# Performance work log

Measured on AMD Instinct MI355X. Metric: run time of the kernel, lower is better.

Reference implementation:

```python
import jax, jax.numpy as jnp
import numpy as np

B, D, NR, H = 8, 64, 6, 3        # batch, input_dim, num_relation, num_hop
R2 = 2 * NR                      # relations incl. inverses
NUM_RULE = R2 ** H               # 1728 combinatorial rules
EPS = 1e-6
TAU = 1.0


def _rule_indices():
    # torch.meshgrid (indexing='ij') over num_hop copies of arange(2*NR), stacked on last dim
    a = np.arange(R2)
    grids = np.meshgrid(*([a] * H), indexing="ij")
    return jnp.asarray(np.stack(grids, -1).reshape(-1, H))  # [NUM_RULE, H] int


def setup_inputs() -> dict:
    key = jax.random.key(0)
    ks = jax.random.split(key, 11)
    s = 0.1
    return {
        "query": jax.random.normal(ks[0], (B, D), jnp.float32),
        "relation_emb": jax.random.normal(ks[1], (R2, D), jnp.float32) * s,      # nn.Embedding(2*NR, D)
        "indicator": jax.random.normal(ks[2], (D,), jnp.float32) * s,            # nn.Embedding(1, D)
        "rel_W": jax.random.normal(ks[3], (H, D, R2 * D), jnp.float32) * s,      # per-layer relation_linear
        "rel_b": jax.random.normal(ks[4], (H, R2 * D), jnp.float32) * s,
        "lin_W": jax.random.normal(ks[5], (H, 13 * D, D), jnp.float32) * s,      # per-layer combine Linear(13D->D)
        "lin_b": jax.random.normal(ks[6], (H, D), jnp.float32) * s,
        "mlp_W1": jax.random.normal(ks[7], (2 * D, D), jnp.float32) * s,
        "mlp_b1": jax.random.normal(ks[8], (D,), jnp.float32) * s,
        "mlp_W2": jax.random.normal(ks[9], (D, 1), jnp.float32) * s,
        "mlp_b2": jax.random.normal(ks[10], (1,), jnp.float32) * s,
    }


def reference(query, relation_emb, indicator, rel_W, rel_b, lin_W, lin_b,
              mlp_W1, mlp_b1, mlp_W2, mlp_b2):
    rel_idx = _rule_indices()                       # [R, H]
    Rn = rel_idx.shape[0]

    # PNA degree scales: each graph is a chain; degree_out+1 (boundary self-message)
    # node 0 -> 1 message (boundary only), nodes 1..H -> 2 messages (edge + boundary)
    log_deg_head = jnp.log(jnp.float32(1.0))
    log_deg_tail = jnp.log(jnp.float32(2.0))
    mean_scale = (log_deg_head + H * log_deg_tail) / (H + 1)
    s_head = log_deg_head / mean_scale
    s_tail = log_deg_tail / mean_scale
    scales_head = jnp.stack([jnp.float32(1.0), s_head, 1.0 / jnp.maximum(s_head, 1e-2)])
    scales_tail = jnp.stack([jnp.float32(1.0), s_tail, 1.0 / jnp.maximum(s_tail, 1e-2)])

    # node-0 PNA update: single message == boundary == indicator (constant across graphs)
    # stats layout per feature dim: (mean, max, min, std)
    f0 = jnp.stack([indicator, indicator, indicator,
                    jnp.full((D,), float(np.sqrt(EPS)), indicator.dtype)], -1).reshape(4 * D)
    upd0 = (f0[:, None] * scales_head).reshape(12 * D)

    # boundary / initial hidden: indicator at node 0 of every graph
    hidden = jnp.zeros((B, Rn, H + 1, D), query.dtype)
    hidden = hidden.at[:, :, 0, :].set(indicator)

    for l in range(H):
        # dependent relation table from the query (relation_linear)
        rel_table = (query @ rel_W[l] + rel_b[l]).reshape(B, R2, D)
        rel = rel_table[:, rel_idx]                 # [B, R, H, D] gather per edge
        msg = hidden[:, :, :-1, :] * rel            # distmult message on edges h -> h+1
        # tail-node PNA stats over message set {msg, boundary=0}
        mean = msg * 0.5
        mx = jnp.maximum(msg, 0.0)
        mn = jnp.minimum(msg, 0.0)
        std = jnp.sqrt(jnp.maximum(msg * msg * 0.25, EPS))   # sq_mean - mean^2 = msg^2/4
        feats = jnp.stack([mean, mx, mn, std], -1).reshape(B, Rn, H, 4 * D)
        upd_tail = (feats[..., None] * scales_tail).reshape(B, Rn, H, 12 * D)
        upd = jnp.concatenate(
            [jnp.broadcast_to(upd0, (B, Rn, 1, 12 * D)), upd_tail], axis=2)
        # combine: relu(Linear(cat([input, update])))
        hidden = jax.nn.relu(
            jnp.concatenate([hidden, upd], -1) @ lin_W[l] + lin_b[l])

    # readout at tail node H, concat per-node query
    feat = jnp.concatenate(
        [hidden[:, :, H, :], jnp.broadcast_to(query[:, None, :], (B, Rn, D))], -1)
    score = (jax.nn.relu(feat @ mlp_W1 + mlp_b1) @ mlp_W2 + mlp_b2)[..., 0]   # [B, R]
    attention = jax.nn.softmax(score / TAU, axis=-1)
    r_emb = relation_emb[rel_idx]                   # [R, H, D]
    subgoals = jnp.einsum("br,rhd->bhd", attention, r_emb)
    masks = jnp.ones((B, H), bool)
    return subgoals, masks
```

## Files before the change

### kernel.cpp

```cpp
#include <hip/hip_runtime.h>
#include <hip/hip_bf16.h>


typedef const float* fp;

#define WS_WT     0
#define WS_RELT   49152
#define WS_QW1    67584
#define WS_Q2     68096
#define WS_QW3    141824
#define WS_SCORES 142592

__device__ __forceinline__ void accq(float4 mv, float4 tv,
                                     float4 wa, float4 wb, float4 wc, float4 wd,
                                     float& acc){
  acc += mv.x*wa.x; acc += fabsf(mv.x)*wa.y; acc += tv.x*wa.z;
  acc += mv.y*wb.x; acc += fabsf(mv.y)*wb.y; acc += tv.y*wb.z;
  acc += mv.z*wc.x; acc += fabsf(mv.z)*wc.y; acc += tv.z*wc.z;
  acc += mv.w*wd.x; acc += fabsf(mv.w)*wd.y; acc += tv.w*wd.z;
}

__global__ void k_pre1(fp lin_W, fp query, fp rel_W, fp rel_b, fp mlp_W1,
                       fp mlp_b1, float* ws){
  int t = blockIdx.x*256 + threadIdx.x;
  if (t < 49152){
    int c = t & 3; int j = (t>>2)&63; int d = (t>>8)&63; int l = t>>14;
    fp W = lin_W + (size_t)l*832*64 + (64 + 12*d)*64 + j;
    float v = 0.f;
    if (c == 0){
      float w0 = W[0]   + (4.f/3.f)*W[64]  + 0.75f*W[128];
      float w1 = W[192] + (4.f/3.f)*W[256] + 0.75f*W[320];
      float w2 = W[384] + (4.f/3.f)*W[448] + 0.75f*W[512];
      v = 0.5f*w0 + 0.5f*(w1 + w2);
    } else if (c == 1){
      float w1 = W[192] + (4.f/3.f)*W[256] + 0.75f*W[320];
      float w2 = W[384] + (4.f/3.f)*W[448] + 0.75f*W[512];
      v = 0.5f*(w1 - w2);
    } else if (c == 2){
      v = 0.5f*(W[576] + (4.f/3.f)*W[640] + 0.75f*W[704]);
    }
    ws[WS_WT + t] = v;
  } else if (t < 67584){
    int e = t - 49152;
    int d = e & 63; int j = (e>>6)%12; int b = (e/768)&7; int l = e/6144;
    float acc = rel_b[l*768 + j*64 + d];
    fp W = rel_W + (size_t)l*64*768 + j*64 + d;
    fp q = query + b*64;
    #pragma unroll 32
    for (int k=0;k<64;k++) acc += q[k] * W[k*768];
    ws[WS_RELT + e] = acc;
  } else if (t < 68096){
    int e = t - 67584; int b = e>>6; int j = e&63;
    float acc = mlp_b1[j];
    fp q = query + b*64;
    #pragma unroll 32
    for (int i=0;i<64;i++) acc += q[i] * mlp_W1[(64+i)*64 + j];
    ws[WS_QW1 + e] = acc;
  }
}

__global__ void k_mid(fp indicator, fp lin_W, fp lin_b, float* ws){
  __shared__ float sC2[64], sC2W[64], sP1[64], sQ3[12][64];
  __shared__ __align__(16) float mP[64], tP[64];
  __shared__ __align__(16) float mL[12][64], tL[12][64];
  int tid = threadIdx.x;
  int w = tid>>6, j = tid&63;
  bool isQ2 = blockIdx.x < 96;
  int b  = isQ2 ? blockIdx.x/12 : blockIdx.x-96;
  int i0 = isQ2 ? blockIdx.x%12 : 0;
  if (w == 0){
    float acc = lin_b[j];
    #pragma unroll 8
    for (int d=0; d<64; d++) acc += 2e-3f * ws[WS_WT + ((d<<6)+j)*4 + 2];
    sC2[j] = fmaxf(acc, 0.f);
  } else if (w == 1 && isQ2){
    const float* rel = ws + WS_RELT + (b*12+i0)*64;
    float m = indicator[j] * rel[j];
    mP[j] = m; tP[j] = fmaxf(fabsf(m), 2e-3f);
  }
  __syncthreads();
  if (w == 0){
    float a2 = lin_b[64+j];
    fp W1 = lin_W + 832*64;
    #pragma unroll 16
    for (int k=0;k<64;k++) a2 += sC2[k] * W1[k*64+j];
    sC2W[j] = a2;
  } else if (w == 1 && isQ2){
    const float4* W4 = (const float4*)(ws + WS_WT);
    float acc = lin_b[j];
    #pragma unroll
    for (int dq=0; dq<16; dq++){
      float4 mv = ((const float4*)mP)[dq], tv = ((const float4*)tP)[dq];
      float4 wa = W4[(dq*4+0)*64+j], wb = W4[(dq*4+1)*64+j],
             wc = W4[(dq*4+2)*64+j], wd = W4[(dq*4+3)*64+j];
      accq(mv,tv,wa,wb,wc,wd,acc);
    }
    sP1[j] = fmaxf(acc, 0.f);
  }
  __syncthreads();
  {
    const float* rel = ws + WS_RELT + 6144 + (b*12+w)*64;
    float s = isQ2 ? sP1[j] : sC2[j];
    float m = s * rel[j];
    mL[w][j] = m; tL[w][j] = fmaxf(fabsf(m), 2e-3f);
  }
  __syncthreads();
  const float4* W4 = (const float4*)(ws + WS_WT + 16384);
  float acc = sC2W[j];
  #pragma unroll
  for (int dq=0; dq<16; dq++){
    float4 mv = ((const float4*)mL[w])[dq], tv = ((const float4*)tL[w])[dq];
    float4 wa = W4[(dq*4+0)*64+j], wb = W4[(dq*4+1)*64+j],
           wc = W4[(dq*4+2)*64+j], wd = W4[(dq*4+3)*64+j];
    accq(mv,tv,wa,wb,wc,wd,acc);
  }
  if (isQ2){
    ws[WS_Q2 + ((b*12+i0)*12+w)*64 + j] = fmaxf(acc, 0.f);
  } else {
    sQ3[w][j] = fmaxf(acc, 0.f);
    __syncthreads();
    fp W2 = lin_W + 2*832*64;
    float a = lin_b[128+j];
    #pragma unroll 16
    for (int k=0;k<64;k++) a += sQ3[w][k]*W2[k*64+j];
    ws[WS_QW3 + (b*12+w)*64 + j] = a;
  }
}

__global__ __launch_bounds__(256) void k_score(fp mlp_W1, fp mlp_W2, float* ws){
  __shared__ float wt_s[4096];
  __shared__ float fin[4][4][64];
  __shared__ __align__(16) float m_s[4][4][64];
  __shared__ __align__(16) float t_s[4][4][64];
  int tid = threadIdx.x, w = tid>>6, j = tid&63;
  int wave = blockIdx.x*4 + w;
  int b = blockIdx.x/108;
  int rem = wave%432;
  int i0 = rem/36; int t36 = rem%36;
  int i2 = t36/3;  int i1b = (t36%3)*4;
  {
    float rl = ws[WS_RELT + 12288 + (b*12+i2)*64 + j];
    #pragma unroll
    for (int r=0;r<4;r++){
      float qv = ws[WS_Q2 + ((b*12+i0)*12 + i1b + r)*64 + j];
      float m = qv*rl;
      m_s[w][r][j] = m;
      t_s[w][r][j] = fmaxf(fabsf(m), 2e-3f);
    }
  }
  float a0 = ws[WS_QW3 + (b*12+i2)*64 + j];
  float acc[4] = {a0, a0, a0, a0};
  const float4* Wt2 = (const float4*)(ws + WS_WT + 32768);
  for (int ch=0; ch<4; ch++){
    __syncthreads();
    {
      const float4* src = Wt2 + ch*1024;
      float4* dst = (float4*)wt_s;
      #pragma unroll
      for (int k=0; k<4; k++) dst[tid + k*256] = src[tid + k*256];
    }
    __syncthreads();
    #pragma unroll
    for (int dq=0; dq<4; dq++){
      int dc = ch*4 + dq;
      const float4* wl = (const float4*)wt_s + dq*256 + j;
      float4 wa = wl[0], wb = wl[64], wc = wl[128], wd = wl[192];
      #pragma unroll
      for (int r=0;r<4;r++){
        float4 mv = ((const float4*)m_s[w][r])[dc];
        float4 tv = ((const float4*)t_s[w][r])[dc];
        accq(mv,tv,wa,wb,wc,wd,acc[r]);
      }
    }
  }
  __syncthreads();
  fin[w][0][j]=fmaxf(acc[0],0.f); fin[w][1][j]=fmaxf(acc[1],0.f);
  fin[w][2][j]=fmaxf(acc[2],0.f); fin[w][3][j]=fmaxf(acc[3],0.f);
  __syncthreads();
  float qw = ws[WS_QW1 + b*64 + j];
  float w2v = mlp_W2[j];
  float h0=qw, h1=qw, h2=qw, h3=qw;
  #pragma unroll 8
  for (int i=0;i<64;i++){
    float wv = mlp_W1[i*64+j];
    h0 += fin[w][0][i]*wv; h1 += fin[w][1][i]*wv;
    h2 += fin[w][2][i]*wv; h3 += fin[w][3][i]*wv;
  }
  float s0=fmaxf(h0,0.f)*w2v, s1=fmaxf(h1,0.f)*w2v;
  float s2=fmaxf(h2,0.f)*w2v, s3=fmaxf(h3,0.f)*w2v;
  #pragma unroll
  for (int off=32; off>0; off>>=1){
    s0 += __shfl_down(s0, off, 64); s1 += __shfl_down(s1, off, 64);
    s2 += __shfl_down(s2, off, 64); s3 += __shfl_down(s3, off, 64);
  }
  if (j == 0){
    int rbase = i0*144 + i1b*12 + i2;
    float* S = ws + WS_SCORES + b*1728 + rbase;
    S[0] = s0; S[12] = s1; S[24] = s2; S[36] = s3;
  }
}

__global__ void k_final(fp relation_emb, float* ws, float* out){
  int b = blockIdx.x, tid = threadIdx.x;
  int w = tid>>6, lane = tid&63;
  __shared__ float se[1728];
  __shared__ float wred[4];
  __shared__ float pb[36][4];
  __shared__ float bins[36];
  const float* sc = ws + WS_SCORES + b*1728;
  float mx = -1e30f;
  for (int r=tid; r<1728; r+=256){ float v = sc[r]; se[r] = v; mx = fmaxf(mx, v); }
  #pragma unroll
  for (int off=32; off>0; off>>=1) mx = fmaxf(mx, __shfl_xor(mx, off, 64));
  if (lane == 0) wred[w] = mx;
  __syncthreads();
  mx = fmaxf(fmaxf(wred[0],wred[1]), fmaxf(wred[2],wred[3]));
  __syncthreads();
  float ts = 0.f;
  for (int r=tid; r<1728; r+=256){ float e = __expf(se[r]-mx); se[r] = e; ts += e; }
  #pragma unroll
  for (int off=32; off>0; off>>=1) ts += __shfl_xor(ts, off, 64);
  if (lane == 0) wred[w] = ts;
  __syncthreads();
  float tot = (wred[0]+wred[1]) + (wred[2]+wred[3]);
  if (tid < 144){
    int bin = tid>>2, q = tid&3;
    int h = bin/12, jj = bin%12;
    float a = 0.f;
    if (h == 0){
      const float* p = se + jj*144 + q*36;
      #pragma unroll 4
      for (int k=0;k<36;k++) a += p[k];
    } else if (h == 1){
      for (int t=q*36; t<q*36+36; t++) a += se[(t/12)*144 + jj*12 + (t%12)];
    } else {
      for (int t=q*36; t<q*36+36; t++) a += se[(t/12)*144 + (t%12)*12 + jj];
    }
    pb[bin][q] = a;
  }
  __syncthreads();
  if (tid < 36) bins[tid] = (pb[tid][0]+pb[tid][1]) + (pb[tid][2]+pb[tid][3]);
  __syncthreads();
  if (tid < 192){
    int h = tid>>6, d = tid&63;
    float acc = 0.f;
    #pragma unroll
    for (int jj=0; jj<12; jj++) acc += bins[h*12+jj] * relation_emb[jj*64+d];
    out[b*192 + tid] = acc/tot;
  }
  if (tid >= 192 && tid < 195){
    out[1536 + b*3 + (tid-192)] = 1.0f;
  }
}

extern "C" void kernel_launch(void* const* d_in, const int* in_sizes, int n_in,
                              void* d_out, int out_size, void* d_ws, size_t ws_size,
                              hipStream_t stream){
  fp query        = (fp)d_in[0];
  fp relation_emb = (fp)d_in[1];
  fp indicator    = (fp)d_in[2];
  fp rel_W        = (fp)d_in[3];
  fp rel_b        = (fp)d_in[4];
  fp lin_W        = (fp)d_in[5];
  fp lin_b        = (fp)d_in[6];
  fp mlp_W1       = (fp)d_in[7];
  fp mlp_b1       = (fp)d_in[8];
  fp mlp_W2       = (fp)d_in[9];
  float* ws = (float*)d_ws;
  float* out = (float*)d_out;

  k_pre1 <<<266, 256, 0, stream>>>(lin_W, query, rel_W, rel_b, mlp_W1, mlp_b1, ws);
  k_mid  <<<104, 768, 0, stream>>>(indicator, lin_W, lin_b, ws);
  k_score<<<864, 256, 0, stream>>>(mlp_W1, mlp_W2, ws);
  k_final<<<8,   256, 0, stream>>>(relation_emb, ws, out);
}
```

Before: 115.5 us.

## Fuse preprocessing and mid kernels, recomputing folded weights per block in LDS

Merges the weight-folding and relation-projection pre-kernel into the mid kernel. Each of the 104 mid blocks now recomputes the folded layer-0/1 weights (32K floats) and its own relation projections into shared memory, while 30 extra blocks produce the layer-2 data that later kernels still read from the workspace. This removes one launch and the global round trip between the two kernels. In exchange it adds redundant global reads and folding work in every block and uses 128KB of LDS per block, which limits occupancy.

After: 145.2 us. 1.26x slower.

```diff
diff --git a/kernel.cpp b/kernel.cpp
--- a/kernel.cpp
+++ b/kernel.cpp
@@ -20,62 +20,96 @@
   acc += mv.w*wd.x; acc += fabsf(mv.w)*wd.y; acc += tv.w*wd.z;
 }
 
-__global__ void k_pre1(fp lin_W, fp query, fp rel_W, fp rel_b, fp mlp_W1,
-                       fp mlp_b1, float* ws){
-  int t = blockIdx.x*256 + threadIdx.x;
-  if (t < 49152){
-    int c = t & 3; int j = (t>>2)&63; int d = (t>>8)&63; int l = t>>14;
-    fp W = lin_W + (size_t)l*832*64 + (64 + 12*d)*64 + j;
-    float v = 0.f;
-    if (c == 0){
-      float w0 = W[0]   + (4.f/3.f)*W[64]  + 0.75f*W[128];
-      float w1 = W[192] + (4.f/3.f)*W[256] + 0.75f*W[320];
-      float w2 = W[384] + (4.f/3.f)*W[448] + 0.75f*W[512];
-      v = 0.5f*w0 + 0.5f*(w1 + w2);
-    } else if (c == 1){
-      float w1 = W[192] + (4.f/3.f)*W[256] + 0.75f*W[320];
-      float w2 = W[384] + (4.f/3.f)*W[448] + 0.75f*W[512];
-      v = 0.5f*(w1 - w2);
-    } else if (c == 2){
-      v = 0.5f*(W[576] + (4.f/3.f)*W[640] + 0.75f*W[704]);
-    }
-    ws[WS_WT + t] = v;
-  } else if (t < 67584){
-    int e = t - 49152;
-    int d = e & 63; int j = (e>>6)%12; int b = (e/768)&7; int l = e/6144;
-    float acc = rel_b[l*768 + j*64 + d];
-    fp W = rel_W + (size_t)l*64*768 + j*64 + d;
+__device__ __forceinline__ float foldWt(fp lin_W, int l, int d, int j, int c){
+  fp W = lin_W + (size_t)l*832*64 + (64 + 12*d)*64 + j;
+  float v = 0.f;
+  if (c == 0){
+    float w0 = W[0]   + (4.f/3.f)*W[64]  + 0.75f*W[128];
+    float w1 = W[192] + (4.f/3.f)*W[256] + 0.75f*W[320];
+    float w2 = W[384] + (4.f/3.f)*W[448] + 0.75f*W[512];
+    v = 0.5f*w0 + 0.5f*(w1 + w2);
+  } else if (c == 1){
+    float w1 = W[192] + (4.f/3.f)*W[256] + 0.75f*W[320];
+    float w2 = W[384] + (4.f/3.f)*W[448] + 0.75f*W[512];
+    v = 0.5f*(w1 - w2);
+  } else if (c == 2){
+    v = 0.5f*(W[576] + (4.f/3.f)*W[640] + 0.75f*W[704]);
+  }
+  return v;
+}
+
+__global__ __launch_bounds__(768) void k_pre(fp indicator, fp query, fp lin_W,
+                       fp lin_b, fp rel_W, fp rel_b, fp mlp_W1, fp mlp_b1,
+                       float* ws){
+  __shared__ float sWt[32768];
+  __shared__ float sC2[64], sC2W[64], sP1[64], sQ3[12][64];
+  __shared__ __align__(16) float mP[64], tP[64];
+  __shared__ __align__(16) float mL[12][64], tL[12][64];
+  __shared__ __align__(16) float sRel0[64];
+  __shared__ __align__(16) float sRel1[12][64];
+  int tid = threadIdx.x;
+
+  if (blockIdx.x < 30){
+    int t = blockIdx.x*768 + tid;
+    if (t < 16384){
+      int g = 32768 + t;
+      int c = g & 3; int j = (g>>2)&63; int d = (g>>8)&63;
+      ws[WS_WT + g] = foldWt(lin_W, 2, d, j, c);
+    } else if (t < 22528){
+      int e = 12288 + (t - 16384);
+      int d = e & 63; int j = (e>>6)%12; int b = (e/768)&7;
+      float acc = rel_b[2*768 + j*64 + d];
+      fp W = rel_W + (size_t)2*64*768 + j*64 + d;
+      fp q = query + b*64;
+      #pragma unroll 32
+      for (int k=0;k<64;k++) acc += q[k] * W[k*768];
+      ws[WS_RELT + e] = acc;
+    } else if (t < 23040){
+      int e = t - 22528; int b = e>>6; int j = e&63;
+      float acc = mlp_b1[j];
+      fp q = query + b*64;
+      #pragma unroll 32
+      for (int i=0;i<64;i++) acc += q[i] * mlp_W1[(64+i)*64 + j];
+      ws[WS_QW1 + e] = acc;
+    }
+    return;
+  }
+
+  int mb = blockIdx.x - 30;
+  int w = tid>>6, j = tid&63;
+  bool isQ2 = mb < 96;
+  int b  = isQ2 ? mb/12 : mb-96;
+  int i0 = isQ2 ? mb%12 : 0;
+
+  for (int f = tid; f < 32768; f += 768){
+    int c = f & 3; int jj = (f>>2)&63; int d = (f>>8)&63; int l = f>>14;
+    sWt[f] = foldWt(lin_W, l, d, jj, c);
+  }
+  {
+    int idx = tid>>6, d = tid&63;
+    float acc = rel_b[768 + idx*64 + d];
+    fp W = rel_W + (size_t)64*768 + idx*64 + d;
     fp q = query + b*64;
     #pragma unroll 32
     for (int k=0;k<64;k++) acc += q[k] * W[k*768];
-    ws[WS_RELT + e] = acc;
-  } else if (t < 68096){
-    int e = t - 67584; int b = e>>6; int j = e&63;
-    float acc = mlp_b1[j];
+    sRel1[idx][d] = acc;
+  }
+  if (isQ2 && tid < 64){
+    float acc = rel_b[i0*64 + tid];
+    fp W = rel_W + i0*64 + tid;
     fp q = query + b*64;
     #pragma unroll 32
-    for (int i=0;i<64;i++) acc += q[i] * mlp_W1[(64+i)*64 + j];
-    ws[WS_QW1 + e] = acc;
-  }
-}
-
-__global__ void k_mid(fp indicator, fp lin_W, fp lin_b, float* ws){
-  __shared__ float sC2[64], sC2W[64], sP1[64], sQ3[12][64];
-  __shared__ __align__(16) float mP[64], tP[64];
-  __shared__ __align__(16) float mL[12][64], tL[12][64];
-  int tid = threadIdx.x;
-  int w = tid>>6, j = tid&63;
-  bool isQ2 = blockIdx.x < 96;
-  int b  = isQ2 ? blockIdx.x/12 : blockIdx.x-96;
-  int i0 = isQ2 ? blockIdx.x%12 : 0;
+    for (int k=0;k<64;k++) acc += q[k] * W[k*768];
+    sRel0[tid] = acc;
+  }
+  __syncthreads();
   if (w == 0){
     float acc = lin_b[j];
     #pragma unroll 8
-    for (int d=0; d<64; d++) acc += 2e-3f * ws[WS_WT + ((d<<6)+j)*4 + 2];
+    for (int d=0; d<64; d++) acc += 2e-3f * sWt[((d<<6)+j)*4 + 2];
     sC2[j] = fmaxf(acc, 0.f);
   } else if (w == 1 && isQ2){
-    const float* rel = ws + WS_RELT + (b*12+i0)*64;
-    float m = indicator[j] * rel[j];
+    float m = indicator[j] * sRel0[j];
     mP[j] = m; tP[j] = fmaxf(fabsf(m), 2e-3f);
   }
   __syncthreads();
@@ -86,7 +120,7 @@
     for (int k=0;k<64;k++) a2 += sC2[k] * W1[k*64+j];
     sC2W[j] = a2;
   } else if (w == 1 && isQ2){
-    const float4* W4 = (const float4*)(ws + WS_WT);
+    const float4* W4 = (const float4*)sWt;
     float acc = lin_b[j];
     #pragma unroll
     for (int dq=0; dq<16; dq++){
@@ -99,13 +133,12 @@
   }
   __syncthreads();
   {
-    const float* rel = ws + WS_RELT + 6144 + (b*12+w)*64;
     float s = isQ2 ? sP1[j] : sC2[j];
-    float m = s * rel[j];
+    float m = s * sRel1[w][j];
     mL[w][j] = m; tL[w][j] = fmaxf(fabsf(m), 2e-3f);
   }
   __syncthreads();
-  const float4* W4 = (const float4*)(ws + WS_WT + 16384);
+  const float4* W4 = (const float4*)(sWt + 16384);
   float acc = sC2W[j];
   #pragma unroll
   for (int dq=0; dq<16; dq++){
@@ -269,8 +302,8 @@
   float* ws = (float*)d_ws;
   float* out = (float*)d_out;
 
-  k_pre1 <<<266, 256, 0, stream>>>(lin_W, query, rel_W, rel_b, mlp_W1, mlp_b1, ws);
-  k_mid  <<<104, 768, 0, stream>>>(indicator, lin_W, lin_b, ws);
+  k_pre  <<<134, 768, 0, stream>>>(indicator, query, lin_W, lin_b, rel_W, rel_b,
+                                   mlp_W1, mlp_b1, ws);
   k_score<<<864, 256, 0, stream>>>(mlp_W1, mlp_W2, ws);
   k_final<<<8,   256, 0, stream>>>(relation_emb, ws, out);
 }
```

## Restructure k_pre1: stage lin_W in shared memory and split-K dot products

Applied to the files above, without the earlier changes.

The weight-folding part of k_pre1 now loads a contiguous lin_W slab into shared memory with float4 loads and computes the folded weights from LDS, instead of doing strided global reads per thread. The rel_W and mlp_W1 query projections are split over four K-chunks per block with a shared-memory reduction, shortening each thread's serial 64-long dot product and raising the block count. This preprocessing kernel is a small part of a 4-kernel pipeline, so it mainly targets latency on the critical path, at the cost of extra syncs and more blocks.

New measurement: 114.7 us. About the same (-0.8%).

```diff
diff --git a/kernel.cpp b/kernel.cpp
--- a/kernel.cpp
+++ b/kernel.cpp
@@ -20,42 +20,66 @@
   acc += mv.w*wd.x; acc += fabsf(mv.w)*wd.y; acc += tv.w*wd.z;
 }
 
-__global__ void k_pre1(fp lin_W, fp query, fp rel_W, fp rel_b, fp mlp_W1,
-                       fp mlp_b1, float* ws){
-  int t = blockIdx.x*256 + threadIdx.x;
-  if (t < 49152){
-    int c = t & 3; int j = (t>>2)&63; int d = (t>>8)&63; int l = t>>14;
-    fp W = lin_W + (size_t)l*832*64 + (64 + 12*d)*64 + j;
-    float v = 0.f;
-    if (c == 0){
-      float w0 = W[0]   + (4.f/3.f)*W[64]  + 0.75f*W[128];
-      float w1 = W[192] + (4.f/3.f)*W[256] + 0.75f*W[320];
-      float w2 = W[384] + (4.f/3.f)*W[448] + 0.75f*W[512];
-      v = 0.5f*w0 + 0.5f*(w1 + w2);
-    } else if (c == 1){
-      float w1 = W[192] + (4.f/3.f)*W[256] + 0.75f*W[320];
-      float w2 = W[384] + (4.f/3.f)*W[448] + 0.75f*W[512];
-      v = 0.5f*(w1 - w2);
-    } else if (c == 2){
-      v = 0.5f*(W[576] + (4.f/3.f)*W[640] + 0.75f*W[704]);
-    }
-    ws[WS_WT + t] = v;
-  } else if (t < 67584){
-    int e = t - 49152;
-    int d = e & 63; int j = (e>>6)%12; int b = (e/768)&7; int l = e/6144;
-    float acc = rel_b[l*768 + j*64 + d];
-    fp W = rel_W + (size_t)l*64*768 + j*64 + d;
-    fp q = query + b*64;
-    #pragma unroll 32
-    for (int k=0;k<64;k++) acc += q[k] * W[k*768];
-    ws[WS_RELT + e] = acc;
-  } else if (t < 68096){
-    int e = t - 67584; int b = e>>6; int j = e&63;
-    float acc = mlp_b1[j];
-    fp q = query + b*64;
-    #pragma unroll 32
-    for (int i=0;i<64;i++) acc += q[i] * mlp_W1[(64+i)*64 + j];
-    ws[WS_QW1 + e] = acc;
+__global__ __launch_bounds__(256) void k_pre1(fp lin_W, fp query, fp rel_W,
+                       fp rel_b, fp mlp_W1, fp mlp_b1, float* ws){
+  __shared__ float sW[3072];
+  __shared__ float part[4][64];
+  int bi = blockIdx.x, tid = threadIdx.x;
+
+  if (bi < 48){
+    int l = bi>>4, d0 = (bi&15)*4;
+    fp src = lin_W + (size_t)l*832*64 + (size_t)(64 + 12*d0)*64;
+    float4* s4 = (float4*)sW;
+    const float4* g4 = (const float4*)src;
+    s4[tid] = g4[tid]; s4[tid+256] = g4[tid+256]; s4[tid+512] = g4[tid+512];
+    __syncthreads();
+    int c = tid&3, j = tid>>2;
+    #pragma unroll
+    for (int dd=0; dd<4; dd++){
+      const float* W = sW + dd*768 + j;
+      float v = 0.f;
+      if (c == 0){
+        float w0 = W[0]   + (4.f/3.f)*W[64]  + 0.75f*W[128];
+        float w1 = W[192] + (4.f/3.f)*W[256] + 0.75f*W[320];
+        float w2 = W[384] + (4.f/3.f)*W[448] + 0.75f*W[512];
+        v = 0.5f*w0 + 0.5f*(w1 + w2);
+      } else if (c == 1){
+        float w1 = W[192] + (4.f/3.f)*W[256] + 0.75f*W[320];
+        float w2 = W[384] + (4.f/3.f)*W[448] + 0.75f*W[512];
+        v = 0.5f*(w1 - w2);
+      } else if (c == 2){
+        v = 0.5f*(W[576] + (4.f/3.f)*W[640] + 0.75f*W[704]);
+      }
+      ws[WS_WT + l*16384 + (d0+dd)*256 + tid] = v;
+    }
+  } else if (bi < 336){
+    int idx = bi - 48;
+    int l = idx/96; int rem = idx%96; int b = rem/12; int jj = rem%12;
+    int d = tid&63, kc = tid>>6;
+    fp W = rel_W + (size_t)l*64*768 + (size_t)(kc*16)*768 + jj*64 + d;
+    fp q = query + b*64 + kc*16;
+    float acc = (kc == 0) ? rel_b[l*768 + jj*64 + d] : 0.f;
+    #pragma unroll
+    for (int k=0;k<16;k++) acc += q[k] * W[k*768];
+    part[kc][d] = acc;
+    __syncthreads();
+    if (tid < 64){
+      float v = ((part[0][tid] + part[1][tid]) + part[2][tid]) + part[3][tid];
+      ws[WS_RELT + l*6144 + b*768 + jj*64 + tid] = v;
+    }
+  } else {
+    int b = bi - 336;
+    int j = tid&63, kc = tid>>6;
+    float acc = (kc == 0) ? mlp_b1[j] : 0.f;
+    fp q = query + b*64 + kc*16;
+    #pragma unroll
+    for (int i=0;i<16;i++) acc += q[i] * mlp_W1[(64 + kc*16 + i)*64 + j];
+    part[kc][j] = acc;
+    __syncthreads();
+    if (tid < 64){
+      float v = ((part[0][tid] + part[1][tid]) + part[2][tid]) + part[3][tid];
+      ws[WS_QW1 + b*64 + tid] = v;
+    }
   }
 }
 
@@ -269,7 +293,7 @@
   float* ws = (float*)d_ws;
   float* out = (float*)d_out;
 
-  k_pre1 <<<266, 256, 0, stream>>>(lin_W, query, rel_W, rel_b, mlp_W1, mlp_b1, ws);
+  k_pre1 <<<344, 256, 0, stream>>>(lin_W, query, rel_W, rel_b, mlp_W1, mlp_b1, ws);
   k_mid  <<<104, 768, 0, stream>>>(indicator, lin_W, lin_b, ws);
   k_score<<<864, 256, 0, stream>>>(mlp_W1, mlp_W2, ws);
   k_final<<<8,   256, 0, stream>>>(relation_emb, ws, out);
```
